# Performance work log

Hardware: AMD Instinct MI355X
Metric: run time of the kernel (lower is better)

The kernel has to match this reference:

```python
import jax, jax.numpy as jnp
import numpy as np

NOISE_LEVEL = 0.02
CROSSTALK = 0.05
COHERENCE = 0.03
HIDDEN = 2048


def _crosstalk_kernel(n):
    # K[i, j] = 1 / (i - j)^2 for i != j, 0 on the diagonal
    idx = jnp.arange(n, dtype=jnp.float32)
    dist = jnp.abs(idx[:, None] - idx[None, :])
    return jnp.where(dist > 0, 1.0 / (dist * dist), 0.0)


def setup_inputs() -> dict:
    key = jax.random.key(0)
    ks = jax.random.split(key, 7)
    B, D_in, H, D_out = 8192, 1024, 2048, 2
    x = jax.random.normal(ks[0], (B, D_in), dtype=jnp.float32)
    # torch nn.Linear-like init scale: 1/sqrt(fan_in)
    W1 = jax.random.normal(ks[1], (H, D_in), dtype=jnp.float32) / np.sqrt(D_in)
    b1 = jax.random.normal(ks[2], (H,), dtype=jnp.float32) / np.sqrt(D_in)
    W2 = jax.random.normal(ks[3], (H, H), dtype=jnp.float32) / np.sqrt(H)
    b2 = jax.random.normal(ks[4], (H,), dtype=jnp.float32) / np.sqrt(H)
    Wout = jax.random.normal(ks[5], (D_out, H), dtype=jnp.float32) / np.sqrt(H)
    bout = jax.random.normal(ks[6], (D_out,), dtype=jnp.float32) / np.sqrt(H)
    return {"x": x, "W1": W1, "b1": b1, "W2": W2, "b2": b2, "Wout": Wout, "bout": bout}


def reference(x, W1, b1, W2, b2, Wout, bout):
    K = _crosstalk_kernel(HIDDEN)
    thermal = jnp.zeros((HIDDEN,), dtype=x.dtype)  # thermal_state buffer, carries across layers
    nkey = jax.random.key(42)

    x = jnp.tanh(x)
    for li, (W, b) in enumerate([(W1, b1), (W2, b2)]):
        x = jnp.tanh(x @ W.T + b)
        # physical noise (add_noise=True, training mode)
        k_noise = jax.random.fold_in(nkey, 2 * li)
        k_phase = jax.random.fold_in(nkey, 2 * li + 1)
        x = x + jax.random.normal(k_noise, x.shape, x.dtype) * NOISE_LEVEL
        # thermal crosstalk: EMA of per-neuron absolute power, then
        # distance-weighted (1/d^2) coupling — the O(n^2) python loop as a matvec
        layer_thermal = jnp.sum(jnp.abs(x), axis=0) * CROSSTALK  # [H]
        thermal = 0.7 * thermal + 0.3 * layer_thermal
        thermal_noise = (thermal @ K) * CROSSTALK  # [H], constant across batch
        x = x + thermal_noise[None, :]
        # coherence (phase-dependent interference)
        phase = jax.random.normal(k_phase, x.shape, x.dtype) * COHERENCE
        x = x + (x * jnp.cos(phase) - x) * COHERENCE
    return x @ Wout.T + bout
```

## Files before the change

### kernel.cpp

```cpp
#include <hip/hip_runtime.h>
#include <stdint.h>
#include <math.h>

#define NOISE_LEVEL 0.02f
#define CROSSTALK   0.05f
#define COHERENCE   0.03f

typedef _Float16 half8 __attribute__((ext_vector_type(8)));
typedef _Float16 half4 __attribute__((ext_vector_type(4)));
typedef __attribute__((ext_vector_type(4))) float f32x4;

#define TF_ROUND(x0,x1,R) { x0 += x1; x1 = ((x1 << (R)) | (x1 >> (32-(R)))); x1 ^= x0; }

__host__ __device__ inline void threefry2x32(uint32_t k0, uint32_t k1,
                                             uint32_t x0, uint32_t x1,
                                             uint32_t& o0, uint32_t& o1)
{
  uint32_t ks2 = k0 ^ k1 ^ 0x1BD11BDAu;
  x0 += k0; x1 += k1;
  TF_ROUND(x0,x1,13) TF_ROUND(x0,x1,15) TF_ROUND(x0,x1,26) TF_ROUND(x0,x1,6)
  x0 += k1; x1 += ks2 + 1u;
  TF_ROUND(x0,x1,17) TF_ROUND(x0,x1,29) TF_ROUND(x0,x1,16) TF_ROUND(x0,x1,24)
  x0 += ks2; x1 += k0 + 2u;
  TF_ROUND(x0,x1,13) TF_ROUND(x0,x1,15) TF_ROUND(x0,x1,26) TF_ROUND(x0,x1,6)
  x0 += k0; x1 += k1 + 3u;
  TF_ROUND(x0,x1,17) TF_ROUND(x0,x1,29) TF_ROUND(x0,x1,16) TF_ROUND(x0,x1,24)
  x0 += k1; x1 += ks2 + 4u;
  TF_ROUND(x0,x1,13) TF_ROUND(x0,x1,15) TF_ROUND(x0,x1,26) TF_ROUND(x0,x1,6)
  o0 = x0 + ks2; o1 = x1 + k0 + 5u;
}

__device__ inline uint32_t jax_bits(uint32_t k0, uint32_t k1, uint32_t idx)
{
  uint32_t o0, o1; threefry2x32(k0, k1, 0u, idx, o0, o1); return o0 ^ o1;
}

__device__ inline float jax_normal(uint32_t k0, uint32_t k1, uint32_t idx)
{
  uint32_t bits = jax_bits(k0, k1, idx);
  float f = __uint_as_float((bits >> 9) | 0x3f800000u) - 1.0f;
  float u = fmaf(f, 2.0f, -0.99999994f);
  u = fmaxf(-0.99999994f, u);
  float w = -__logf(fmaf(-u, u, 1.0f));
  float p;
  if (w < 5.0f) {
    w -= 2.5f;
    p = 2.81022636e-08f;
    p = fmaf(p, w, 3.43273939e-07f);
    p = fmaf(p, w, -3.5233877e-06f);
    p = fmaf(p, w, -4.39150654e-06f);
    p = fmaf(p, w, 0.00021858087f);
    p = fmaf(p, w, -0.00125372503f);
    p = fmaf(p, w, -0.00417768164f);
    p = fmaf(p, w, 0.246640727f);
    p = fmaf(p, w, 1.50140941f);
  } else {
    w = sqrtf(w) - 3.0f;
    p = -0.000200214257f;
    p = fmaf(p, w, 0.000100950558f);
    p = fmaf(p, w, 0.00134934322f);
    p = fmaf(p, w, -0.00367342844f);
    p = fmaf(p, w, 0.00573950773f);
    p = fmaf(p, w, -0.0076224613f);
    p = fmaf(p, w, 0.00943887047f);
    p = fmaf(p, w, 1.00167406f);
    p = fmaf(p, w, 2.83297682f);
  }
  return 1.41421354f * (p * u);
}

__device__ inline float cos_small(float p)
{
  float p2 = p * p;
  return 1.0f + p2 * (-0.5f + p2 * (4.16666679e-02f + p2 * (-1.38888892e-03f)));
}

__device__ inline float tanh_fast(float x)
{
  float ax = fabsf(x);
  float e = __expf(2.0f * ax);
  float r = 1.0f - 2.0f / (e + 1.0f);
  return copysignf(r, x);
}


__global__ __launch_bounds__(256)
void pack_plane(const float* __restrict__ in, _Float16* __restrict__ out,
                int R, int K, int kshift, int do_tanh)
{
  const int nslots = R * (K >> 3);
  const int ktm = (K >> 6) - 1;
  int g = blockIdx.x * 256 + threadIdx.x;
  const int stride = gridDim.x * 256;
  for (; g < nslots; g += stride) {
    int tile = g >> 10;
    int s = g & 1023;
    int kq = s >> 7, row = s & 127;
    int rb = tile >> kshift, kt = tile & ktm;
    int r = rb * 128 + row;
    int k = kt * 64 + kq * 8;
    const float* src = in + (size_t)r * K + k;
    float4 v0 = *(const float4*)src;
    float4 v1 = *(const float4*)(src + 4);
    float xs[8] = {v0.x, v0.y, v0.z, v0.w, v1.x, v1.y, v1.z, v1.w};
    half8 h;
    #pragma unroll
    for (int e = 0; e < 8; ++e) {
      float x = do_tanh ? tanh_fast(xs[e]) : xs[e];
      h[e] = (_Float16)x;
    }
    *(half8*)&out[(size_t)g * 8] = h;
  }
}

__device__ __forceinline__ size_t cnat_idx(int r, int c)
{
  int bm = r >> 7, bn = c >> 7, rr = r & 127, cc = c & 127;
  int w = ((rr >> 6) << 1) | (cc >> 6);
  int fm = (rr >> 4) & 3, lg = (rr >> 2) & 3, j = rr & 3;
  int fn = (cc >> 4) & 3, lm = cc & 15;
  return (((size_t)(bm * 16 + bn) * 4 + w) * 4096)
         + (size_t)(fn * 16 + fm * 4 + j) * 64 + lg * 16 + lm;
}

__global__ __launch_bounds__(256)
void coherence_pack_small(const _Float16* __restrict__ xn, const float* __restrict__ tn,
                          _Float16* __restrict__ out,
                          uint32_t pk0, uint32_t pk1, int R, int K, int kshift)
{
  const int nslots = R * (K >> 3);
  const int ktm = (K >> 6) - 1;
  int g = blockIdx.x * 256 + threadIdx.x;
  const int stride = gridDim.x * 256;
  for (; g < nslots; g += stride) {
    int tile = g >> 10;
    int s = g & 1023;
    int kq = s >> 7, row = s & 127;
    int rb = tile >> kshift, kt = tile & ktm;
    int r = rb * 128 + row;
    int k = kt * 64 + kq * 8;
    half8 xv = *(const half8*)&xn[cnat_idx(r, k)];
    float4 t0 = *(const float4*)&tn[k];
    float4 t1 = *(const float4*)&tn[k + 4];
    float ts[8] = {t0.x, t0.y, t0.z, t0.w, t1.x, t1.y, t1.z, t1.w};
    uint32_t fb = (uint32_t)(r * K + k);
    half8 h;
    #pragma unroll
    for (int e = 0; e < 8; ++e) {
      float vv = (float)xv[e] + ts[e];
      float ph = COHERENCE * jax_normal(pk0, pk1, fb + e);
      float cp = cos_small(ph);
      float xvv = vv + (vv * cp - vv) * COHERENCE;
      h[e] = (_Float16)(xvv - ts[e]);
    }
    *(half8*)&out[(size_t)g * 8] = h;
  }
}

__global__ __launch_bounds__(256)
void bias_fold(const float* __restrict__ tn, const float* __restrict__ W,
               const float* __restrict__ b, float* __restrict__ fold, int K)
{
  const int wid = threadIdx.x >> 6;
  const int lane = threadIdx.x & 63;
  const int j = blockIdx.x * 4 + wid;
  const float* row = W + (size_t)j * K;
  float s = 0.0f;
  for (int h = lane; h < K; h += 64) s = fmaf(tn[h], row[h], s);
  #pragma unroll
  for (int off = 32; off > 0; off >>= 1) s += __shfl_down(s, off);
  if (lane == 0) fold[j] = b[j] + s;
}

#define BM 128
#define BN 128
#define TILEH 8192
#define BUFH  (2 * TILEH)

__device__ __forceinline__ f32x4 noise_group(int g, int blockM, int blockN,
                                             int wr, int wc, int lg, int lm,
                                             int N, uint32_t k0, uint32_t k1)
{
  int fn = g >> 2, fm = g & 3;
  int gr0 = blockM + wr * 64 + fm * 16 + lg * 4;
  int gc  = blockN + wc * 64 + fn * 16 + lm;
  f32x4 r;
  #pragma unroll
  for (int j = 0; j < 4; ++j)
    r[j] = jax_normal(k0, k1, (uint32_t)((gr0 + j) * N + gc));
  return r;
}

__global__ __launch_bounds__(256)
void gemm_f16(const _Float16* __restrict__ Ap, const _Float16* __restrict__ Bp,
              const float* __restrict__ bias, _Float16* __restrict__ outn,
              float* __restrict__ colabs, int M, int N, int K,
              uint32_t nk0, uint32_t nk1)
{
  __shared__ __align__(16) _Float16 lds[2 * BUFH];

  const int t = threadIdx.x;
  const int nwg = gridDim.x;
  const int wg = (blockIdx.x & 7) * (nwg >> 3) + (blockIdx.x >> 3);
  const int nbn = N / BN;
  const int bn = wg & (nbn - 1);
  const int bm = wg / nbn;
  const int blockM = bm * BM, blockN = bn * BN;

  const int lane = t & 63;
  const int w = t >> 6;
  const int wr = w >> 1, wc = w & 1;
  const int lm = lane & 15, lg = lane >> 4;

  const int op = w >> 1;
  const int part = w & 1;
  const _Float16* gplane = op ? Bp : Ap;
  const int blk = op ? bn : bm;
  const int ktiles = K >> 6;
  const _Float16* gsrc0 = gplane + ((size_t)blk * ktiles) * TILEH
                          + part * (TILEH / 2) + lane * 8;
  _Float16* lbase = lds + op * TILEH + part * (TILEH / 2);

#define STAGE(buf, kt_) {                                                      \
    _Float16* lp = lbase + (buf) * BUFH;                                       \
    const _Float16* s = gsrc0 + (size_t)(kt_) * TILEH;                         \
    _Pragma("unroll")                                                          \
    for (int i = 0; i < 8; ++i)                                                \
      __builtin_amdgcn_global_load_lds((const void*)(s + i * 512),             \
                                       (void*)(lp + i * 512), 16, 0, 0);       \
  }

  f32x4 acc[4][4];
  #pragma unroll
  for (int i = 0; i < 4; ++i)
    #pragma unroll
    for (int j = 0; j < 4; ++j) acc[i][j] = 0.0f;

  f32x4 nz0 = 0.0f, nz1 = 0.0f, nz2 = 0.0f, nz3 = 0.0f;
  f32x4 nz4 = 0.0f, nz5 = 0.0f, nz6 = 0.0f, nz7 = 0.0f;
  f32x4 nz8 = 0.0f, nz9 = 0.0f, nz10 = 0.0f, nz11 = 0.0f;
  f32x4 nz12 = 0.0f, nz13 = 0.0f, nz14 = 0.0f, nz15 = 0.0f;

  const int nk = ktiles;
  STAGE(0, 0);
  __syncthreads();
  int cur = 0;

  for (int kt = 0; kt < nk; ++kt) {
    if (kt + 1 < nk) STAGE(cur ^ 1, kt + 1);

    const _Float16* base = lds + cur * BUFH;
    #pragma unroll
    for (int ks = 0; ks < 2; ++ks) {
      half8 fa[4], fb[4];
      const int kq = ks * 4 + lg;
      #pragma unroll
      for (int fm = 0; fm < 4; ++fm)
        fa[fm] = *(const half8*)(base + kq * 1024 + (wr * 64 + fm * 16 + lm) * 8);
      #pragma unroll
      for (int fn = 0; fn < 4; ++fn)
        fb[fn] = *(const half8*)(base + TILEH + kq * 1024 + (wc * 64 + fn * 16 + lm) * 8);
      #pragma unroll
      for (int fm = 0; fm < 4; ++fm)
        #pragma unroll
        for (int fn = 0; fn < 4; ++fn)
          acc[fm][fn] = __builtin_amdgcn_mfma_f32_16x16x32_f16(fa[fm], fb[fn], acc[fm][fn], 0, 0, 0);
    }

    if (kt < 16) {
      f32x4 v = noise_group(kt, blockM, blockN, wr, wc, lg, lm, N, nk0, nk1);
      switch (kt) {
        case 0:  nz0  = v; break;  case 1:  nz1  = v; break;
        case 2:  nz2  = v; break;  case 3:  nz3  = v; break;
        case 4:  nz4  = v; break;  case 5:  nz5  = v; break;
        case 6:  nz6  = v; break;  case 7:  nz7  = v; break;
        case 8:  nz8  = v; break;  case 9:  nz9  = v; break;
        case 10: nz10 = v; break;  case 11: nz11 = v; break;
        case 12: nz12 = v; break;  case 13: nz13 = v; break;
        case 14: nz14 = v; break;  default: nz15 = v; break;
      }
    }

    __syncthreads();
    cur ^= 1;
  }

  const size_t obase = (((size_t)(bm * nbn + bn) * 4 + w) * 4096) + lane;

#define EPI_STORE(fm_, fn_, NZV)                                               \
    _Pragma("unroll")                                                          \
    for (int j = 0; j < 4; ++j) {                                              \
      float v = tanh_fast(acc[fm_][fn_][j] + bv) + NOISE_LEVEL * NZV[j];       \
      outn[obase + (size_t)((fn_)*16 + (fm_)*4 + j) * 64] = (_Float16)v;       \
      cp += fabsf(v);                                                          \
    }

#define EPI_FN(fn_, NZA, NZB, NZC, NZD) {                                      \
    const int gc = blockN + wc * 64 + (fn_)*16 + lm;                           \
    const float bv = bias[gc];                                                 \
    float cp = 0.0f;                                                           \
    EPI_STORE(0, fn_, NZA) EPI_STORE(1, fn_, NZB)                              \
    EPI_STORE(2, fn_, NZC) EPI_STORE(3, fn_, NZD)                              \
    cp += __shfl_xor(cp, 16);                                                  \
    cp += __shfl_xor(cp, 32);                                                  \
    if (lg == 0) atomicAdd(&colabs[gc], cp);                                   \
  }

  EPI_FN(0, nz0,  nz1,  nz2,  nz3)
  EPI_FN(1, nz4,  nz5,  nz6,  nz7)
  EPI_FN(2, nz8,  nz9,  nz10, nz11)
  EPI_FN(3, nz12, nz13, nz14, nz15)
#undef EPI_FN
#undef EPI_STORE
#undef STAGE
}

__global__ __launch_bounds__(256)
void thermal_tn(const float* __restrict__ colabs, const float* __restrict__ prev_thermal,
                float* __restrict__ thermal_out, float* __restrict__ tn_out, int has_prev)
{
  __shared__ float th[2048];
  __shared__ float inv[2048];
  const int t = threadIdx.x;
  for (int j = t; j < 2048; j += 256) {
    float lt = colabs[j] * CROSSTALK;
    float pv = has_prev ? prev_thermal[j] : 0.0f;
    th[j] = 0.7f * pv + 0.3f * lt;
    float d = (float)j;
    inv[j] = (j == 0) ? 0.0f : 1.0f / (d * d);
  }
  __syncthreads();
  const int i = blockIdx.x * 256 + t;
  float s = 0.0f;
  #pragma unroll 4
  for (int j = 0; j < 2048; ++j) {
    int d = i - j; d = d < 0 ? -d : d;
    s += th[j] * inv[d];
  }
  tn_out[i] = s * CROSSTALK;
  thermal_out[i] = th[i];
}

__global__ __launch_bounds__(256)
void final_out(const _Float16* __restrict__ a2n, const float* __restrict__ tn2,
               const float* __restrict__ Wout, const float* __restrict__ bout,
               float* __restrict__ out, uint32_t pk0, uint32_t pk1)
{
  const int wave = threadIdx.x >> 6;
  const int lane = threadIdx.x & 63;
  const int b = blockIdx.x * 4 + wave;
  float acc0 = 0.0f, acc1 = 0.0f;
  #pragma unroll
  for (int i = 0; i < 8; ++i) {
    int h = lane * 4 + i * 256;
    half4 v4 = *(const half4*)&a2n[cnat_idx(b, h)];
    float4 tv = *(const float4*)&tn2[h];
    float4 w0 = *(const float4*)&Wout[h];
    float4 w1 = *(const float4*)&Wout[2048 + h];
    float xs[4]  = {(float)v4[0] + tv.x, (float)v4[1] + tv.y,
                    (float)v4[2] + tv.z, (float)v4[3] + tv.w};
    float w0s[4] = {w0.x, w0.y, w0.z, w0.w};
    float w1s[4] = {w1.x, w1.y, w1.z, w1.w};
    uint32_t fb = (uint32_t)(b * 2048 + h);
    #pragma unroll
    for (int e = 0; e < 4; ++e) {
      float ph = COHERENCE * jax_normal(pk0, pk1, fb + e);
      float cp = cos_small(ph);
      float xv = xs[e] + (xs[e] * cp - xs[e]) * COHERENCE;
      acc0 = fmaf(xv, w0s[e], acc0);
      acc1 = fmaf(xv, w1s[e], acc1);
    }
  }
  #pragma unroll
  for (int off = 32; off > 0; off >>= 1) {
    acc0 += __shfl_down(acc0, off);
    acc1 += __shfl_down(acc1, off);
  }
  if (lane == 0) {
    out[(size_t)b * 2 + 0] = acc0 + bout[0];
    out[(size_t)b * 2 + 1] = acc1 + bout[1];
  }
}

extern "C" void kernel_launch(void* const* d_in, const int* in_sizes, int n_in,
                              void* d_out, int out_size, void* d_ws, size_t ws_size,
                              hipStream_t stream)
{
  (void)in_sizes; (void)n_in; (void)out_size; (void)ws_size;
  const float* x    = (const float*)d_in[0];
  const float* W1   = (const float*)d_in[1];
  const float* b1   = (const float*)d_in[2];
  const float* W2   = (const float*)d_in[3];
  const float* b2   = (const float*)d_in[4];
  const float* Wout = (const float*)d_in[5];
  const float* bout = (const float*)d_in[6];
  float* out = (float*)d_out;

  const int M = 8192, H = 2048, Din = 1024;
  const size_t MB = (size_t)1024 * 1024;

  char* ws = (char*)d_ws;
  _Float16* a_nat = (_Float16*)ws;
  _Float16* Apk = (_Float16*)(ws + 32 * MB);
  _Float16* W1p = (_Float16*)(ws + 64 * MB);
  _Float16* W2p = (_Float16*)(ws + 68 * MB);
  float* small = (float*)(ws + 80 * MB);
  float* colabs1  = small + 0 * H;
  float* colabs2  = small + 1 * H;
  float* thermal1 = small + 2 * H;
  float* thermal2 = small + 3 * H;
  float* tn1      = small + 4 * H;
  float* tn2      = small + 5 * H;
  float* foldb    = small + 6 * H;

  uint32_t kn0a, kn0b, kp0a, kp0b, kn1a, kn1b, kp1a, kp1b;
  threefry2x32(0u, 42u, 0u, 0u, kn0a, kn0b);
  threefry2x32(0u, 42u, 0u, 1u, kp0a, kp0b);
  threefry2x32(0u, 42u, 0u, 2u, kn1a, kn1b);
  threefry2x32(0u, 42u, 0u, 3u, kp1a, kp1b);

  hipMemsetAsync(colabs1, 0, 2 * H * sizeof(float), stream);

  pack_plane<<<1024, 256, 0, stream>>>(W1, W1p, H, Din, 4, 0);
  pack_plane<<<2048, 256, 0, stream>>>(W2, W2p, H, H, 5, 0);
  pack_plane<<<2048, 256, 0, stream>>>(x, Apk, M, Din, 4, 1);

  const int nblk = (M / BM) * (H / BN);
  gemm_f16<<<nblk, 256, 0, stream>>>(Apk, W1p, b1, a_nat, colabs1,
                                     M, H, Din, kn0a, kn0b);
  thermal_tn<<<H / 256, 256, 0, stream>>>(colabs1, nullptr, thermal1, tn1, 0);
  bias_fold<<<H / 4, 256, 0, stream>>>(tn1, W2, b2, foldb, H);
  coherence_pack_small<<<2048, 256, 0, stream>>>(a_nat, tn1, Apk,
                                                 kp0a, kp0b, M, H, 5);
  gemm_f16<<<nblk, 256, 0, stream>>>(Apk, W2p, foldb, a_nat, colabs2,
                                     M, H, H, kn1a, kn1b);
  thermal_tn<<<H / 256, 256, 0, stream>>>(colabs2, thermal1, thermal2, tn2, 1);
  final_out<<<M / 4, 256, 0, stream>>>(a_nat, tn2, Wout, bout, out, kp1a, kp1b);
}
```

Before: 430.5 us.

## Halve GEMM K-tile to 32 and make normal sampler tail branch wave-uniform

The GEMM K-tile drops from 64 to 32 halves, which halves the LDS buffers and doubles the number of main-loop iterations. The packing kernels change their tile layout to match. The normal sampler now always evaluates the central polynomial and runs the tail polynomial only when some lane in the wavefront needs it, which avoids divergent branching. The smaller tile may raise occupancy but adds more barriers per K. The noise generation spread over the first 16 iterations now covers a smaller share of the loop.

Measured after the change: 437.4 us. No clear change (+1.6%).

```diff
diff --git a/kernel.cpp b/kernel.cpp
--- a/kernel.cpp
+++ b/kernel.cpp
@@ -42,29 +42,28 @@
   float u = fmaf(f, 2.0f, -0.99999994f);
   u = fmaxf(-0.99999994f, u);
   float w = -__logf(fmaf(-u, u, 1.0f));
-  float p;
-  if (w < 5.0f) {
-    w -= 2.5f;
-    p = 2.81022636e-08f;
-    p = fmaf(p, w, 3.43273939e-07f);
-    p = fmaf(p, w, -3.5233877e-06f);
-    p = fmaf(p, w, -4.39150654e-06f);
-    p = fmaf(p, w, 0.00021858087f);
-    p = fmaf(p, w, -0.00125372503f);
-    p = fmaf(p, w, -0.00417768164f);
-    p = fmaf(p, w, 0.246640727f);
-    p = fmaf(p, w, 1.50140941f);
-  } else {
-    w = sqrtf(w) - 3.0f;
-    p = -0.000200214257f;
-    p = fmaf(p, w, 0.000100950558f);
-    p = fmaf(p, w, 0.00134934322f);
-    p = fmaf(p, w, -0.00367342844f);
-    p = fmaf(p, w, 0.00573950773f);
-    p = fmaf(p, w, -0.0076224613f);
-    p = fmaf(p, w, 0.00943887047f);
-    p = fmaf(p, w, 1.00167406f);
-    p = fmaf(p, w, 2.83297682f);
+  float wl = w - 2.5f;
+  float p = 2.81022636e-08f;
+  p = fmaf(p, wl, 3.43273939e-07f);
+  p = fmaf(p, wl, -3.5233877e-06f);
+  p = fmaf(p, wl, -4.39150654e-06f);
+  p = fmaf(p, wl, 0.00021858087f);
+  p = fmaf(p, wl, -0.00125372503f);
+  p = fmaf(p, wl, -0.00417768164f);
+  p = fmaf(p, wl, 0.246640727f);
+  p = fmaf(p, wl, 1.50140941f);
+  if (__any(w >= 5.0f)) {
+    float ws = sqrtf(w) - 3.0f;
+    float q = -0.000200214257f;
+    q = fmaf(q, ws, 0.000100950558f);
+    q = fmaf(q, ws, 0.00134934322f);
+    q = fmaf(q, ws, -0.00367342844f);
+    q = fmaf(q, ws, 0.00573950773f);
+    q = fmaf(q, ws, -0.0076224613f);
+    q = fmaf(q, ws, 0.00943887047f);
+    q = fmaf(q, ws, 1.00167406f);
+    q = fmaf(q, ws, 2.83297682f);
+    p = (w >= 5.0f) ? q : p;
   }
   return 1.41421354f * (p * u);
 }
@@ -89,16 +88,16 @@
                 int R, int K, int kshift, int do_tanh)
 {
   const int nslots = R * (K >> 3);
-  const int ktm = (K >> 6) - 1;
+  const int ktm = (K >> 5) - 1;
   int g = blockIdx.x * 256 + threadIdx.x;
   const int stride = gridDim.x * 256;
   for (; g < nslots; g += stride) {
-    int tile = g >> 10;
-    int s = g & 1023;
+    int tile = g >> 9;
+    int s = g & 511;
     int kq = s >> 7, row = s & 127;
     int rb = tile >> kshift, kt = tile & ktm;
     int r = rb * 128 + row;
-    int k = kt * 64 + kq * 8;
+    int k = kt * 32 + kq * 8;
     const float* src = in + (size_t)r * K + k;
     float4 v0 = *(const float4*)src;
     float4 v1 = *(const float4*)(src + 4);
@@ -129,16 +128,16 @@
                           uint32_t pk0, uint32_t pk1, int R, int K, int kshift)
 {
   const int nslots = R * (K >> 3);
-  const int ktm = (K >> 6) - 1;
+  const int ktm = (K >> 5) - 1;
   int g = blockIdx.x * 256 + threadIdx.x;
   const int stride = gridDim.x * 256;
   for (; g < nslots; g += stride) {
-    int tile = g >> 10;
-    int s = g & 1023;
+    int tile = g >> 9;
+    int s = g & 511;
     int kq = s >> 7, row = s & 127;
     int rb = tile >> kshift, kt = tile & ktm;
     int r = rb * 128 + row;
-    int k = kt * 64 + kq * 8;
+    int k = kt * 32 + kq * 8;
     half8 xv = *(const half8*)&xn[cnat_idx(r, k)];
     float4 t0 = *(const float4*)&tn[k];
     float4 t1 = *(const float4*)&tn[k + 4];
@@ -174,7 +173,7 @@
 
 #define BM 128
 #define BN 128
-#define TILEH 8192
+#define TILEH 4096
 #define BUFH  (2 * TILEH)
 
 __device__ __forceinline__ f32x4 noise_group(int g, int blockM, int blockN,
@@ -216,7 +215,7 @@
   const int part = w & 1;
   const _Float16* gplane = op ? Bp : Ap;
   const int blk = op ? bn : bm;
-  const int ktiles = K >> 6;
+  const int ktiles = K >> 5;
   const _Float16* gsrc0 = gplane + ((size_t)blk * ktiles) * TILEH
                           + part * (TILEH / 2) + lane * 8;
   _Float16* lbase = lds + op * TILEH + part * (TILEH / 2);
@@ -225,7 +224,7 @@
     _Float16* lp = lbase + (buf) * BUFH;                                       \
     const _Float16* s = gsrc0 + (size_t)(kt_) * TILEH;                         \
     _Pragma("unroll")                                                          \
-    for (int i = 0; i < 8; ++i)                                                \
+    for (int i = 0; i < 4; ++i)                                                \
       __builtin_amdgcn_global_load_lds((const void*)(s + i * 512),             \
                                        (void*)(lp + i * 512), 16, 0, 0);       \
   }
@@ -250,22 +249,18 @@
     if (kt + 1 < nk) STAGE(cur ^ 1, kt + 1);
 
     const _Float16* base = lds + cur * BUFH;
-    #pragma unroll
-    for (int ks = 0; ks < 2; ++ks) {
-      half8 fa[4], fb[4];
-      const int kq = ks * 4 + lg;
-      #pragma unroll
-      for (int fm = 0; fm < 4; ++fm)
-        fa[fm] = *(const half8*)(base + kq * 1024 + (wr * 64 + fm * 16 + lm) * 8);
+    half8 fa[4], fb[4];
+    #pragma unroll
+    for (int fm = 0; fm < 4; ++fm)
+      fa[fm] = *(const half8*)(base + lg * 1024 + (wr * 64 + fm * 16 + lm) * 8);
+    #pragma unroll
+    for (int fn = 0; fn < 4; ++fn)
+      fb[fn] = *(const half8*)(base + TILEH + lg * 1024 + (wc * 64 + fn * 16 + lm) * 8);
+    #pragma unroll
+    for (int fm = 0; fm < 4; ++fm)
       #pragma unroll
       for (int fn = 0; fn < 4; ++fn)
-        fb[fn] = *(const half8*)(base + TILEH + kq * 1024 + (wc * 64 + fn * 16 + lm) * 8);
-      #pragma unroll
-      for (int fm = 0; fm < 4; ++fm)
-        #pragma unroll
-        for (int fn = 0; fn < 4; ++fn)
-          acc[fm][fn] = __builtin_amdgcn_mfma_f32_16x16x32_f16(fa[fm], fb[fn], acc[fm][fn], 0, 0, 0);
-    }
+        acc[fm][fn] = __builtin_amdgcn_mfma_f32_16x16x32_f16(fa[fm], fb[fn], acc[fm][fn], 0, 0, 0);
 
     if (kt < 16) {
       f32x4 v = noise_group(kt, blockM, blockN, wr, wc, lg, lm, N, nk0, nk1);
@@ -421,9 +416,9 @@
 
   hipMemsetAsync(colabs1, 0, 2 * H * sizeof(float), stream);
 
-  pack_plane<<<1024, 256, 0, stream>>>(W1, W1p, H, Din, 4, 0);
-  pack_plane<<<2048, 256, 0, stream>>>(W2, W2p, H, H, 5, 0);
-  pack_plane<<<2048, 256, 0, stream>>>(x, Apk, M, Din, 4, 1);
+  pack_plane<<<1024, 256, 0, stream>>>(W1, W1p, H, Din, 5, 0);
+  pack_plane<<<2048, 256, 0, stream>>>(W2, W2p, H, H, 6, 0);
+  pack_plane<<<2048, 256, 0, stream>>>(x, Apk, M, Din, 5, 1);
 
   const int nblk = (M / BM) * (H / BN);
   gemm_f16<<<nblk, 256, 0, stream>>>(Apk, W1p, b1, a_nat, colabs1,
@@ -431,7 +426,7 @@
   thermal_tn<<<H / 256, 256, 0, stream>>>(colabs1, nullptr, thermal1, tn1, 0);
   bias_fold<<<H / 4, 256, 0, stream>>>(tn1, W2, b2, foldb, H);
   coherence_pack_small<<<2048, 256, 0, stream>>>(a_nat, tn1, Apk,
-                                                 kp0a, kp0b, M, H, 5);
+                                                 kp0a, kp0b, M, H, 6);
   gemm_f16<<<nblk, 256, 0, stream>>>(Apk, W2p, foldb, a_nat, colabs2,
                                      M, H, H, kn1a, kn1b);
   thermal_tn<<<H / 256, 256, 0, stream>>>(colabs2, thermal1, thermal2, tn2, 1);
```
